# Kernel tuning notes

Measured on AMD Instinct MI355X. Metric: run time of the kernel, lower is better.

## Reference

```python
import jax, jax.numpy as jnp
import numpy as np

HIDDEN = 128
GRID = 8
NB = 32.0            # neighborhood_size
CELL = NB / GRID      # cell_size


def setup_inputs() -> dict:
    key = jax.random.key(0)
    k1, k2, k3, k4 = jax.random.split(key, 4)
    N = 1024
    hidden_states = jax.random.normal(k1, (N, HIDDEN), dtype=jnp.float32)
    positions = jax.random.uniform(k2, (N, 2), dtype=jnp.float32) * 100.0
    fan_in = GRID * GRID * HIDDEN
    bound = 1.0 / np.sqrt(fan_in)
    W = jax.random.uniform(k3, (fan_in, HIDDEN), dtype=jnp.float32, minval=-bound, maxval=bound)
    b = jax.random.uniform(k4, (HIDDEN,), dtype=jnp.float32, minval=-bound, maxval=bound)
    return {"hidden_states": hidden_states, "positions": positions, "W": W, "b": b}


def reference(hidden_states, positions, W, b):
    N, H = hidden_states.shape
    G = GRID
    pos = jax.lax.stop_gradient(positions)  # indices carry no gradient (matches torch int())
    # rel[i, j] = positions[j] - positions[i]
    rel = pos[None, :, :] - pos[:, None, :]                      # [N, N, 2]
    half = NB / 2.0
    inside = (jnp.abs(rel[..., 0]) <= half) & (jnp.abs(rel[..., 1]) <= half)
    not_self = ~jnp.eye(N, dtype=bool)
    valid = inside & not_self                                     # [N, N]
    # rel + half is in [0, NB] when inside, so floor == int() truncation
    gx = jnp.clip(jnp.floor((rel[..., 0] + half) / CELL).astype(jnp.int32), 0, G - 1)
    gy = jnp.clip(jnp.floor((rel[..., 1] + half) / CELL).astype(jnp.int32), 0, G - 1)
    cell = gy * G + gx                                            # [N, N], in [0, G*G)
    # invalid pairs go to a dummy cell G*G per pedestrian
    seg = jnp.where(valid, cell, G * G)
    gid = (jnp.arange(N, dtype=jnp.int32)[:, None] * (G * G + 1) + seg).reshape(-1)
    data = jnp.broadcast_to(hidden_states[None, :, :], (N, N, H)).reshape(N * N, H)
    gmax = jax.ops.segment_max(data, gid, num_segments=N * (G * G + 1))  # [N*(G*G+1), H]
    # torch grid starts at zeros and uses maximum -> clamp at 0; empty cells (-inf) -> 0
    grid = jnp.maximum(gmax.reshape(N, G * G + 1, H)[:, : G * G, :], 0.0)  # [N, G*G, H]
    flat = grid.reshape(N, G * G * H)
    return flat @ W + b
```

## Files before the change

### kernel.cpp

```cpp
#include <hip/hip_runtime.h>
#include <hip/hip_bf16.h>

#define N_PED 1024
#define H 128
#define G 8
#define NCELL 64
#define K_TOT 8192
#define HALF_NB 16.0f
#define INV_CELL 0.25f

#define KSPLIT 16
#define KC 512
#define BM 32
#define BK 64

typedef __attribute__((ext_vector_type(8))) short bf16x8;
typedef __attribute__((ext_vector_type(4))) float f32x4;

__device__ __forceinline__ unsigned map_f2u(float v) {
    unsigned u = __float_as_uint(v);
    return (u & 0x80000000u) ? ~u : (u | 0x80000000u);
}
__device__ __forceinline__ float unmap_u2f(unsigned u) {
    return __uint_as_float((u & 0x80000000u) ? (u ^ 0x80000000u) : ~u);
}
__device__ __forceinline__ ushort f2bf(float f) {
    unsigned u = __float_as_uint(f);
    return (ushort)((u + 0x7FFFu + ((u >> 16) & 1u)) >> 16);
}
__device__ __forceinline__ void gl_lds16(const void* g, void* l) {
    __builtin_amdgcn_global_load_lds(
        (const __attribute__((address_space(1))) void*)g,
        (__attribute__((address_space(3))) void*)l, 16, 0, 0);
}

__global__ __launch_bounds__(512) void fused_pre(const float* __restrict__ hs,
                                                 const float* __restrict__ pos,
                                                 const float* __restrict__ W,
                                                 ushort* __restrict__ grid,
                                                 ushort* __restrict__ Wt) {
    __shared__ __align__(16) char smem[36872];
    const int tid = threadIdx.x;

    if (blockIdx.x < N_PED) {
        unsigned* lgrid = (unsigned*)smem;
        int*      list  = (int*)(smem + 32768);
        int*      cnt   = (int*)(smem + 36864);
        const int i = blockIdx.x;

        const unsigned iu = 0x80000000u;
        uint4 iv = {iu, iu, iu, iu};
        for (int k = tid; k < NCELL * H / 4; k += 512) ((uint4*)lgrid)[k] = iv;
        if (tid == 0) *cnt = 0;
        __syncthreads();

        const float2 pi = ((const float2*)pos)[i];
        for (int j = tid; j < N_PED; j += 512) {
            float2 pj = ((const float2*)pos)[j];
            float rx = pj.x - pi.x;
            float ry = pj.y - pi.y;
            if (j != i && fabsf(rx) <= HALF_NB && fabsf(ry) <= HALF_NB) {
                int gx = (int)floorf((rx + HALF_NB) * INV_CELL);
                int gy = (int)floorf((ry + HALF_NB) * INV_CELL);
                gx = min(G - 1, max(0, gx));
                gy = min(G - 1, max(0, gy));
                int slot = atomicAdd(cnt, 1);
                list[slot] = (j << 8) | (gy * G + gx);
            }
        }
        __syncthreads();

        const int n   = *cnt;
        const int dim = tid & 127;
        const int eg  = tid >> 7;
        for (int e = eg; e < n; e += 4) {
            int packed = list[e];
            int j    = packed >> 8;
            int cell = packed & 255;
            float v = hs[j * H + dim];
            atomicMax(&lgrid[cell * H + dim], map_f2u(v));
        }
        __syncthreads();

        ushort* dst = grid + (size_t)i * K_TOT;
        for (int c = tid; c < K_TOT / 8; c += 512) {
            uint4 a = ((const uint4*)lgrid)[2 * c];
            uint4 b = ((const uint4*)lgrid)[2 * c + 1];
            ushort tmp[8];
            tmp[0] = f2bf(unmap_u2f(a.x)); tmp[1] = f2bf(unmap_u2f(a.y));
            tmp[2] = f2bf(unmap_u2f(a.z)); tmp[3] = f2bf(unmap_u2f(a.w));
            tmp[4] = f2bf(unmap_u2f(b.x)); tmp[5] = f2bf(unmap_u2f(b.y));
            tmp[6] = f2bf(unmap_u2f(b.z)); tmp[7] = f2bf(unmap_u2f(b.w));
            *(bf16x8*)&dst[8 * c] = *(const bf16x8*)tmp;
        }
    } else {
        float* tile = (float*)smem;
        const int bw  = blockIdx.x - N_PED;
        const int k0w = bw * 64;

        for (int x = tid; x < 64 * H; x += 512) {
            int r = x >> 7, c = x & 127;
            tile[r * 129 + c] = W[(size_t)(k0w + r) * H + c];
        }
        __syncthreads();

        const int col = tid >> 2;
        const int kh  = (tid & 3) * 16;
        ushort tmp[16];
        #pragma unroll
        for (int t = 0; t < 16; ++t) tmp[t] = f2bf(tile[(kh + t) * 129 + col]);
        ushort* w0 = Wt + (size_t)col * K_TOT + k0w + kh;
        *(bf16x8*)w0       = *(const bf16x8*)&tmp[0];
        *(bf16x8*)(w0 + 8) = *(const bf16x8*)&tmp[8];
    }
}

__global__ __launch_bounds__(256) void gemm_mfma(const ushort* __restrict__ A,
                                                 const ushort* __restrict__ Wt,
                                                 float* __restrict__ part) {
    __shared__ ushort sA[BM * BK];
    __shared__ ushort sB[H * BK];

    const int m0   = blockIdx.x * BM;
    const int k0   = blockIdx.y * KC;
    const int tid  = threadIdx.x;
    const int wave = tid >> 6;
    const int lane = tid & 63;
    const int ll   = lane & 15;
    const int lh   = lane >> 4;
    const int lr8  = lane >> 3;
    const int cswz = (lane & 7) ^ (lr8 & 7);

    f32x4 acc[2][2] = {};

    for (int kk = 0; kk < KC; kk += BK) {
        const int kcol = k0 + kk;
        gl_lds16(A + (size_t)(m0 + 8 * wave + lr8) * K_TOT + kcol + cswz * 8,
                 &sA[8 * wave * BK]);
        #pragma unroll
        for (int t = 0; t < 4; ++t) {
            int br = 32 * wave + 8 * t;
            gl_lds16(Wt + (size_t)(br + lr8) * K_TOT + kcol + cswz * 8,
                     &sB[br * BK]);
        }
        __syncthreads();

        #pragma unroll
        for (int ks = 0; ks < 2; ++ks) {
            const int chunk = ks * 4 + lh;
            bf16x8 bfrag[2], afrag[2];
            #pragma unroll
            for (int nt = 0; nt < 2; ++nt) {
                int br = wave * 32 + nt * 16 + ll;
                bfrag[nt] = *(const bf16x8*)&sB[br * BK + ((chunk ^ (br & 7)) * 8)];
            }
            #pragma unroll
            for (int mt = 0; mt < 2; ++mt) {
                int ar = mt * 16 + ll;
                afrag[mt] = *(const bf16x8*)&sA[ar * BK + ((chunk ^ (ar & 7)) * 8)];
            }
            #pragma unroll
            for (int mt = 0; mt < 2; ++mt)
                #pragma unroll
                for (int nt = 0; nt < 2; ++nt)
                    acc[mt][nt] = __builtin_amdgcn_mfma_f32_16x16x32_bf16(
                        afrag[mt], bfrag[nt], acc[mt][nt], 0, 0, 0);
        }
        __syncthreads();
    }

    float* dst = part + (size_t)blockIdx.y * (N_PED * H);
    #pragma unroll
    for (int mt = 0; mt < 2; ++mt)
        #pragma unroll
        for (int nt = 0; nt < 2; ++nt) {
            int col   = wave * 32 + nt * 16 + ll;
            int rbase = m0 + mt * 16 + lh * 4;
            #pragma unroll
            for (int r = 0; r < 4; ++r)
                dst[(size_t)(rbase + r) * H + col] = acc[mt][nt][r];
        }
}

__global__ __launch_bounds__(128) void reduce_out(const float* __restrict__ part,
                                                  const float* __restrict__ b,
                                                  float* __restrict__ out) {
    const int idx = (blockIdx.x * 128 + threadIdx.x) * 4;
    float4 acc = *(const float4*)&b[idx & (H - 1)];
    #pragma unroll
    for (int s = 0; s < KSPLIT; ++s) {
        float4 p = *(const float4*)&part[(size_t)s * (N_PED * H) + idx];
        acc.x += p.x; acc.y += p.y; acc.z += p.z; acc.w += p.w;
    }
    *(float4*)&out[idx] = acc;
}

extern "C" void kernel_launch(void* const* d_in, const int* in_sizes, int n_in,
                              void* d_out, int out_size, void* d_ws, size_t ws_size,
                              hipStream_t stream) {
    const float* hs  = (const float*)d_in[0];
    const float* pos = (const float*)d_in[1];
    const float* Wm  = (const float*)d_in[2];
    const float* b   = (const float*)d_in[3];
    float* out = (float*)d_out;

    ushort* grid = (ushort*)d_ws;
    ushort* Wt   = (ushort*)((char*)d_ws + (16u << 20));
    float*  part = (float*)((char*)d_ws + (18u << 20));

    fused_pre<<<N_PED + K_TOT / 64, 512, 0, stream>>>(hs, pos, Wm, grid, Wt);
    gemm_mfma<<<dim3(N_PED / BM, KSPLIT), 256, 0, stream>>>(grid, Wt, part);
    reduce_out<<<(N_PED * H) / (128 * 4), 128, 0, stream>>>(part, b, out);
}
```

Measured before the change: 32.90 us.

## Triple-buffer GEMM LDS loads and vectorize scatter-max with prefetching

The GEMM kernel now keeps three LDS buffers and issues async global-to-LDS loads two K-steps ahead, waiting on vmcnt counters instead of a full barrier after every tile. The aim is to overlap memory latency with MFMA work. Separately, the scatter-max phase now has each thread handle four feature dims with float4 loads and software-prefetches the next neighbor's list entry and hidden-state row. Risks are higher LDS use per block and hand-written waitcnt logic that must stay in step with the number of loads in flight.

```diff
diff --git a/kernel.cpp b/kernel.cpp
--- a/kernel.cpp
+++ b/kernel.cpp
@@ -13,6 +13,7 @@
 #define KC 512
 #define BM 32
 #define BK 64
+#define NSTAGE 8
 
 typedef __attribute__((ext_vector_type(8))) short bf16x8;
 typedef __attribute__((ext_vector_type(4))) float f32x4;
@@ -70,15 +71,24 @@
         }
         __syncthreads();
 
-        const int n   = *cnt;
-        const int dim = tid & 127;
-        const int eg  = tid >> 7;
-        for (int e = eg; e < n; e += 4) {
-            int packed = list[e];
-            int j    = packed >> 8;
-            int cell = packed & 255;
-            float v = hs[j * H + dim];
-            atomicMax(&lgrid[cell * H + dim], map_f2u(v));
+        const int n    = *cnt;
+        const int dim4 = (tid & 31) * 4;
+        const int eg   = tid >> 5;
+        int e  = eg;
+        int p0 = (e < n) ? list[e] : -1;
+        int p1 = (e + 16 < n) ? list[e + 16] : -1;
+        float4 v0 = {};
+        if (p0 >= 0) v0 = *(const float4*)&hs[(p0 >> 8) * H + dim4];
+        while (p0 >= 0) {
+            int p2 = (e + 32 < n) ? list[e + 32] : -1;
+            float4 v1 = {};
+            if (p1 >= 0) v1 = *(const float4*)&hs[(p1 >> 8) * H + dim4];
+            unsigned* gph = &lgrid[(p0 & 255) * H + dim4];
+            atomicMax(gph + 0, map_f2u(v0.x));
+            atomicMax(gph + 1, map_f2u(v0.y));
+            atomicMax(gph + 2, map_f2u(v0.z));
+            atomicMax(gph + 3, map_f2u(v0.w));
+            e += 16; p0 = p1; p1 = p2; v0 = v1;
         }
         __syncthreads();
 
@@ -118,8 +128,8 @@
 __global__ __launch_bounds__(256) void gemm_mfma(const ushort* __restrict__ A,
                                                  const ushort* __restrict__ Wt,
                                                  float* __restrict__ part) {
-    __shared__ ushort sA[BM * BK];
-    __shared__ ushort sB[H * BK];
+    __shared__ ushort sA[3][BM * BK];
+    __shared__ ushort sB[3][H * BK];
 
     const int m0   = blockIdx.x * BM;
     const int k0   = blockIdx.y * KC;
@@ -131,20 +141,30 @@
     const int lr8  = lane >> 3;
     const int cswz = (lane & 7) ^ (lr8 & 7);
 
+    const ushort* Abase = A  + (size_t)(m0 + 8 * wave + lr8) * K_TOT + k0 + cswz * 8;
+    const ushort* Bbase = Wt + (size_t)(32 * wave + lr8) * K_TOT      + k0 + cswz * 8;
+
     f32x4 acc[2][2] = {};
 
-    for (int kk = 0; kk < KC; kk += BK) {
-        const int kcol = k0 + kk;
-        gl_lds16(A + (size_t)(m0 + 8 * wave + lr8) * K_TOT + kcol + cswz * 8,
-                 &sA[8 * wave * BK]);
-        #pragma unroll
-        for (int t = 0; t < 4; ++t) {
-            int br = 32 * wave + 8 * t;
-            gl_lds16(Wt + (size_t)(br + lr8) * K_TOT + kcol + cswz * 8,
-                     &sB[br * BK]);
-        }
-        __syncthreads();
-
+#define STAGE(T, BUF)                                                        \
+    do {                                                                     \
+        gl_lds16(Abase + (T) * BK, &sA[BUF][8 * wave * BK]);                 \
+        gl_lds16(Bbase + (T) * BK,                &sB[BUF][(32 * wave) * BK]);      \
+        gl_lds16(Bbase + (T) * BK +  8 * K_TOT,   &sB[BUF][(32 * wave + 8) * BK]);  \
+        gl_lds16(Bbase + (T) * BK + 16 * K_TOT,   &sB[BUF][(32 * wave + 16) * BK]); \
+        gl_lds16(Bbase + (T) * BK + 24 * K_TOT,   &sB[BUF][(32 * wave + 24) * BK]); \
+    } while (0)
+
+    STAGE(0, 0);
+    STAGE(1, 1);
+    asm volatile("s_waitcnt vmcnt(5)" ::: "memory");
+    __builtin_amdgcn_s_barrier();
+
+    #pragma unroll
+    for (int t = 0; t < NSTAGE; ++t) {
+        if (t + 2 < NSTAGE) STAGE(t + 2, (t + 2) % 3);
+
+        const int buf = t % 3;
         #pragma unroll
         for (int ks = 0; ks < 2; ++ks) {
             const int chunk = ks * 4 + lh;
@@ -152,12 +172,12 @@
             #pragma unroll
             for (int nt = 0; nt < 2; ++nt) {
                 int br = wave * 32 + nt * 16 + ll;
-                bfrag[nt] = *(const bf16x8*)&sB[br * BK + ((chunk ^ (br & 7)) * 8)];
+                bfrag[nt] = *(const bf16x8*)&sB[buf][br * BK + ((chunk ^ (br & 7)) * 8)];
             }
             #pragma unroll
             for (int mt = 0; mt < 2; ++mt) {
                 int ar = mt * 16 + ll;
-                afrag[mt] = *(const bf16x8*)&sA[ar * BK + ((chunk ^ (ar & 7)) * 8)];
+                afrag[mt] = *(const bf16x8*)&sA[buf][ar * BK + ((chunk ^ (ar & 7)) * 8)];
             }
             #pragma unroll
             for (int mt = 0; mt < 2; ++mt)
@@ -166,8 +186,16 @@
                     acc[mt][nt] = __builtin_amdgcn_mfma_f32_16x16x32_bf16(
                         afrag[mt], bfrag[nt], acc[mt][nt], 0, 0, 0);
         }
-        __syncthreads();
+
+        if (t + 1 < NSTAGE) {
+            if (t + 2 < NSTAGE)
+                asm volatile("s_waitcnt vmcnt(5)" ::: "memory");
+            else
+                asm volatile("s_waitcnt vmcnt(0)" ::: "memory");
+            __builtin_amdgcn_s_barrier();
+        }
     }
+#undef STAGE
 
     float* dst = part + (size_t)blockIdx.y * (N_PED * H);
     #pragma unroll
```

Measured after the change: 30.17 us. 8.3% less time.

## Fuse grid max-pooling into GEMM and replace split-K reduction with atomics

Applied to the files above, without the earlier changes.

Rather than building a full bf16 grid tensor in global memory, the prep kernel now only writes per-pedestrian neighbor lists, the bf16 transpose of W, and a bias-initialized output. The GEMM kernel filters each list to its 4-cell K-chunk, builds that slice of the pooled grid in LDS with atomicMax, and runs MFMA with triple-buffered B loads. Results are accumulated into the output with float atomics, which removes the separate reduce kernel, the partial-sum buffer and the 16 MB grid round-trip. In exchange, neighbor lists are capped (256 per pedestrian, 2048 per block), which silently drops neighbors if exceeded. The atomic summation also makes the output order nondeterministic, and the GEMM now needs about 147 KB of LDS per block.

```diff
diff --git a/kernel.cpp b/kernel.cpp
--- a/kernel.cpp
+++ b/kernel.cpp
@@ -4,15 +4,11 @@
 #define N_PED 1024
 #define H 128
 #define G 8
-#define NCELL 64
 #define K_TOT 8192
 #define HALF_NB 16.0f
 #define INV_CELL 0.25f
-
-#define KSPLIT 16
-#define KC 512
-#define BM 32
-#define BK 64
+#define LISTCAP 256
+#define MLISTCAP 2048
 
 typedef __attribute__((ext_vector_type(8))) short bf16x8;
 typedef __attribute__((ext_vector_type(4))) float f32x4;
@@ -34,76 +30,26 @@
         (__attribute__((address_space(3))) void*)l, 16, 0, 0);
 }
 
-__global__ __launch_bounds__(512) void fused_pre(const float* __restrict__ hs,
-                                                 const float* __restrict__ pos,
-                                                 const float* __restrict__ W,
-                                                 ushort* __restrict__ grid,
-                                                 ushort* __restrict__ Wt) {
-    __shared__ __align__(16) char smem[36872];
+__global__ __launch_bounds__(512) void prep(const float* __restrict__ hs,
+                                            const float* __restrict__ pos,
+                                            const float* __restrict__ W,
+                                            const float* __restrict__ b,
+                                            ushort* __restrict__ Wt,
+                                            int* __restrict__ lists,
+                                            int* __restrict__ cntg,
+                                            float* __restrict__ out) {
+    __shared__ __align__(16) char smem[33168];
     const int tid = threadIdx.x;
-
-    if (blockIdx.x < N_PED) {
-        unsigned* lgrid = (unsigned*)smem;
-        int*      list  = (int*)(smem + 32768);
-        int*      cnt   = (int*)(smem + 36864);
-        const int i = blockIdx.x;
-
-        const unsigned iu = 0x80000000u;
-        uint4 iv = {iu, iu, iu, iu};
-        for (int k = tid; k < NCELL * H / 4; k += 512) ((uint4*)lgrid)[k] = iv;
-        if (tid == 0) *cnt = 0;
-        __syncthreads();
-
-        const float2 pi = ((const float2*)pos)[i];
-        for (int j = tid; j < N_PED; j += 512) {
-            float2 pj = ((const float2*)pos)[j];
-            float rx = pj.x - pi.x;
-            float ry = pj.y - pi.y;
-            if (j != i && fabsf(rx) <= HALF_NB && fabsf(ry) <= HALF_NB) {
-                int gx = (int)floorf((rx + HALF_NB) * INV_CELL);
-                int gy = (int)floorf((ry + HALF_NB) * INV_CELL);
-                gx = min(G - 1, max(0, gx));
-                gy = min(G - 1, max(0, gy));
-                int slot = atomicAdd(cnt, 1);
-                list[slot] = (j << 8) | (gy * G + gx);
-            }
-        }
-        __syncthreads();
-
-        const int n   = *cnt;
-        const int dim = tid & 127;
-        const int eg  = tid >> 7;
-        for (int e = eg; e < n; e += 4) {
-            int packed = list[e];
-            int j    = packed >> 8;
-            int cell = packed & 255;
-            float v = hs[j * H + dim];
-            atomicMax(&lgrid[cell * H + dim], map_f2u(v));
-        }
-        __syncthreads();
-
-        ushort* dst = grid + (size_t)i * K_TOT;
-        for (int c = tid; c < K_TOT / 8; c += 512) {
-            uint4 a = ((const uint4*)lgrid)[2 * c];
-            uint4 b = ((const uint4*)lgrid)[2 * c + 1];
-            ushort tmp[8];
-            tmp[0] = f2bf(unmap_u2f(a.x)); tmp[1] = f2bf(unmap_u2f(a.y));
-            tmp[2] = f2bf(unmap_u2f(a.z)); tmp[3] = f2bf(unmap_u2f(a.w));
-            tmp[4] = f2bf(unmap_u2f(b.x)); tmp[5] = f2bf(unmap_u2f(b.y));
-            tmp[6] = f2bf(unmap_u2f(b.z)); tmp[7] = f2bf(unmap_u2f(b.w));
-            *(bf16x8*)&dst[8 * c] = *(const bf16x8*)tmp;
-        }
-    } else {
+    const int bx  = blockIdx.x;
+
+    if (bx < 128) {
         float* tile = (float*)smem;
-        const int bw  = blockIdx.x - N_PED;
-        const int k0w = bw * 64;
-
+        const int k0w = bx * 64;
         for (int x = tid; x < 64 * H; x += 512) {
             int r = x >> 7, c = x & 127;
             tile[r * 129 + c] = W[(size_t)(k0w + r) * H + c];
         }
         __syncthreads();
-
         const int col = tid >> 2;
         const int kh  = (tid & 3) * 16;
         ushort tmp[16];
@@ -112,87 +58,171 @@
         ushort* w0 = Wt + (size_t)col * K_TOT + k0w + kh;
         *(bf16x8*)w0       = *(const bf16x8*)&tmp[0];
         *(bf16x8*)(w0 + 8) = *(const bf16x8*)&tmp[8];
-    }
-}
-
-__global__ __launch_bounds__(256) void gemm_mfma(const ushort* __restrict__ A,
-                                                 const ushort* __restrict__ Wt,
-                                                 float* __restrict__ part) {
-    __shared__ ushort sA[BM * BK];
-    __shared__ ushort sB[H * BK];
-
-    const int m0   = blockIdx.x * BM;
-    const int k0   = blockIdx.y * KC;
-    const int tid  = threadIdx.x;
-    const int wave = tid >> 6;
-    const int lane = tid & 63;
-    const int ll   = lane & 15;
-    const int lh   = lane >> 4;
+    } else if (bx < 160) {
+        float2* pis   = (float2*)smem;
+        int*    lcnt  = (int*)(smem + 256);
+        int*    llist = (int*)(smem + 384);
+        const int base = (bx - 128) * 32;
+        if (tid < 32) { pis[tid] = ((const float2*)pos)[base + tid]; lcnt[tid] = 0; }
+        __syncthreads();
+        for (int j = tid; j < N_PED; j += 512) {
+            float2 pj = ((const float2*)pos)[j];
+            #pragma unroll
+            for (int p = 0; p < 32; ++p) {
+                float rx = pj.x - pis[p].x;
+                float ry = pj.y - pis[p].y;
+                if (j != base + p && fabsf(rx) <= HALF_NB && fabsf(ry) <= HALF_NB) {
+                    int gx = min(G - 1, max(0, (int)floorf((rx + HALF_NB) * INV_CELL)));
+                    int gy = min(G - 1, max(0, (int)floorf((ry + HALF_NB) * INV_CELL)));
+                    int slot = atomicAdd(&lcnt[p], 1);
+                    if (slot < LISTCAP) llist[p * LISTCAP + slot] = (j << 8) | (gy * G + gx);
+                }
+            }
+        }
+        __syncthreads();
+        for (int x = tid; x < 32 * 64; x += 512)
+            ((int4*)lists)[base * 64 + x] = ((const int4*)llist)[x];
+        if (tid < 32) cntg[base + tid] = min(lcnt[tid], LISTCAP);
+    } else {
+        const float4* b4 = (const float4*)b;
+        float4* out4 = (float4*)out;
+        const int b0 = (bx - 160) * 16384;
+        for (int i = tid; i < 16384; i += 512) {
+            int g = b0 + i;
+            out4[g] = b4[g & 31];
+        }
+    }
+}
+
+__global__ __launch_bounds__(512) void gemm_fused(const float* __restrict__ hs,
+                                                  const ushort* __restrict__ Wt,
+                                                  const int* __restrict__ lists,
+                                                  const int* __restrict__ cntg,
+                                                  float* __restrict__ out) {
+    __shared__ __align__(16) char smem[147600];
+    ushort* Alds  = (ushort*)smem;
+    int*    mlist = (int*)smem;
+    uint*   P     = (uint*)(smem + 32768);
+    ushort* Blds  = (ushort*)(smem + 98304);
+    int*    mcnt  = (int*)(smem + 147456);
+    int*    scnt  = (int*)(smem + 147460);
+
+    const int tid = threadIdx.x;
+    const int m0  = blockIdx.x * 32;
+    const int cy  = blockIdx.y;
+
+    const int wave = tid >> 6, lane = tid & 63;
+    const int ll = lane & 15, lh = lane >> 4;
     const int lr8  = lane >> 3;
     const int cswz = (lane & 7) ^ (lr8 & 7);
-
-    f32x4 acc[2][2] = {};
-
-    for (int kk = 0; kk < KC; kk += BK) {
-        const int kcol = k0 + kk;
-        gl_lds16(A + (size_t)(m0 + 8 * wave + lr8) * K_TOT + kcol + cswz * 8,
-                 &sA[8 * wave * BK]);
-        #pragma unroll
-        for (int t = 0; t < 4; ++t) {
-            int br = 32 * wave + 8 * t;
-            gl_lds16(Wt + (size_t)(br + lr8) * K_TOT + kcol + cswz * 8,
-                     &sB[br * BK]);
-        }
-        __syncthreads();
-
+    const ushort* B0 = Wt + (size_t)(16 * wave + lr8) * K_TOT + cy * 512 + cswz * 8;
+
+#define STAGE(T, BUF)                                                         \
+    do {                                                                      \
+        gl_lds16(B0 + (T) * 64,             Blds + (BUF) * 8192 + (16 * wave) * 64);     \
+        gl_lds16(B0 + (T) * 64 + 8 * K_TOT, Blds + (BUF) * 8192 + (16 * wave + 8) * 64); \
+    } while (0)
+
+    STAGE(0, 0);
+    STAGE(1, 1);
+
+    {
+        uint4 iv = {0x80000000u, 0x80000000u, 0x80000000u, 0x80000000u};
+        uint4* P4 = (uint4*)P;
+        for (int i = tid; i < 4096; i += 512) P4[i] = iv;
+        if (tid == 0) *mcnt = 0;
+        if (tid < 32) scnt[tid] = cntg[m0 + tid];
+    }
+    __syncthreads();
+
+    for (int x = tid; x < 32 * 64; x += 512) {
+        int p = x >> 6, q = x & 63;
+        int4 v = ((const int4*)(lists + (size_t)(m0 + p) * LISTCAP))[q];
+        int n = scnt[p];
+        int e0 = q * 4;
+        int vv[4] = {v.x, v.y, v.z, v.w};
+        #pragma unroll
+        for (int i = 0; i < 4; ++i) {
+            if (e0 + i < n) {
+                int pk = vv[i];
+                int cell = pk & 255;
+                if ((cell >> 2) == cy) {
+                    int slot = atomicAdd(mcnt, 1);
+                    if (slot < MLISTCAP)
+                        mlist[slot] = ((pk >> 8) << 7) | (p << 2) | (cell & 3);
+                }
+            }
+        }
+    }
+    __syncthreads();
+
+    const int mc = min(*mcnt, MLISTCAP);
+    const float4* hs4 = (const float4*)hs;
+    for (int u = tid; u < mc * 32; u += 512) {
+        int m = u >> 5, f = u & 31;
+        int pk = mlist[m];
+        int j = pk >> 7, p = (pk >> 2) & 31, c = pk & 3;
+        float4 v = hs4[j * 32 + f];
+        uint* q = P + p * 512 + c * 128 + f * 4;
+        atomicMax(q + 0, map_f2u(v.x));
+        atomicMax(q + 1, map_f2u(v.y));
+        atomicMax(q + 2, map_f2u(v.z));
+        atomicMax(q + 3, map_f2u(v.w));
+    }
+    __syncthreads();
+
+    for (int x = tid; x < 2048; x += 512) {
+        int r = x >> 6, c = x & 63;
+        const uint* src = P + r * 512 + c * 8;
+        ushort tmp[8];
+        #pragma unroll
+        for (int i = 0; i < 8; ++i) tmp[i] = f2bf(unmap_u2f(src[i]));
+        *(bf16x8*)&Alds[r * 512 + (c ^ (r & 7)) * 8] = *(const bf16x8*)tmp;
+    }
+
+    const int mt = wave >> 2;
+    const int nq = wave & 3;
+
+    f32x4 acc[2] = {};
+
+    asm volatile("s_waitcnt vmcnt(2)" ::: "memory");
+    __syncthreads();
+
+    #pragma unroll
+    for (int t = 0; t < 8; ++t) {
+        if (t + 2 < 8) STAGE(t + 2, (t + 2) % 3);
+        const ushort* Bb = Blds + (t % 3) * 8192;
         #pragma unroll
         for (int ks = 0; ks < 2; ++ks) {
-            const int chunk = ks * 4 + lh;
-            bf16x8 bfrag[2], afrag[2];
+            int ch  = ks * 4 + lh;
+            int gch = t * 8 + ch;
+            bf16x8 bfrag[2];
             #pragma unroll
             for (int nt = 0; nt < 2; ++nt) {
-                int br = wave * 32 + nt * 16 + ll;
-                bfrag[nt] = *(const bf16x8*)&sB[br * BK + ((chunk ^ (br & 7)) * 8)];
+                int br = nq * 32 + nt * 16 + ll;
+                bfrag[nt] = *(const bf16x8*)&Bb[br * 64 + ((ch ^ (br & 7)) * 8)];
             }
-            #pragma unroll
-            for (int mt = 0; mt < 2; ++mt) {
-                int ar = mt * 16 + ll;
-                afrag[mt] = *(const bf16x8*)&sA[ar * BK + ((chunk ^ (ar & 7)) * 8)];
-            }
-            #pragma unroll
-            for (int mt = 0; mt < 2; ++mt)
-                #pragma unroll
-                for (int nt = 0; nt < 2; ++nt)
-                    acc[mt][nt] = __builtin_amdgcn_mfma_f32_16x16x32_bf16(
-                        afrag[mt], bfrag[nt], acc[mt][nt], 0, 0, 0);
-        }
-        __syncthreads();
-    }
-
-    float* dst = part + (size_t)blockIdx.y * (N_PED * H);
+            int ar = mt * 16 + ll;
+            bf16x8 afrag = *(const bf16x8*)&Alds[ar * 512 + ((gch ^ (ar & 7)) * 8)];
+            acc[0] = __builtin_amdgcn_mfma_f32_16x16x32_bf16(afrag, bfrag[0], acc[0], 0, 0, 0);
+            acc[1] = __builtin_amdgcn_mfma_f32_16x16x32_bf16(afrag, bfrag[1], acc[1], 0, 0, 0);
+        }
+        if (t + 1 < 8) {
+            if (t + 2 < 8) asm volatile("s_waitcnt vmcnt(2)" ::: "memory");
+            else           asm volatile("s_waitcnt vmcnt(0)" ::: "memory");
+            __builtin_amdgcn_s_barrier();
+        }
+    }
+#undef STAGE
+
     #pragma unroll
-    for (int mt = 0; mt < 2; ++mt)
-        #pragma unroll
-        for (int nt = 0; nt < 2; ++nt) {
-            int col   = wave * 32 + nt * 16 + ll;
-            int rbase = m0 + mt * 16 + lh * 4;
-            #pragma unroll
-            for (int r = 0; r < 4; ++r)
-                dst[(size_t)(rbase + r) * H + col] = acc[mt][nt][r];
-        }
-}
-
-__global__ __launch_bounds__(128) void reduce_out(const float* __restrict__ part,
-                                                  const float* __restrict__ b,
-                                                  float* __restrict__ out) {
-    const int idx = (blockIdx.x * 128 + threadIdx.x) * 4;
-    float4 acc = *(const float4*)&b[idx & (H - 1)];
-    #pragma unroll
-    for (int s = 0; s < KSPLIT; ++s) {
-        float4 p = *(const float4*)&part[(size_t)s * (N_PED * H) + idx];
-        acc.x += p.x; acc.y += p.y; acc.z += p.z; acc.w += p.w;
-    }
-    *(float4*)&out[idx] = acc;
+    for (int nt = 0; nt < 2; ++nt) {
+        int col = nq * 32 + nt * 16 + ll;
+        int row = m0 + mt * 16 + lh * 4;
+        #pragma unroll
+        for (int r = 0; r < 4; ++r)
+            atomicAdd(&out[(size_t)(row + r) * H + col], acc[nt][r]);
+    }
 }
 
 extern "C" void kernel_launch(void* const* d_in, const int* in_sizes, int n_in,
@@ -204,11 +234,10 @@
     const float* b   = (const float*)d_in[3];
     float* out = (float*)d_out;
 
-    ushort* grid = (ushort*)d_ws;
-    ushort* Wt   = (ushort*)((char*)d_ws + (16u << 20));
-    float*  part = (float*)((char*)d_ws + (18u << 20));
-
-    fused_pre<<<N_PED + K_TOT / 64, 512, 0, stream>>>(hs, pos, Wm, grid, Wt);
-    gemm_mfma<<<dim3(N_PED / BM, KSPLIT), 256, 0, stream>>>(grid, Wt, part);
-    reduce_out<<<(N_PED * H) / (128 * 4), 128, 0, stream>>>(part, b, out);
-}
+    ushort* Wt    = (ushort*)d_ws;
+    int*    lists = (int*)((char*)d_ws + (2u << 20));
+    int*    cntg  = (int*)((char*)d_ws + (3u << 20));
+
+    prep<<<162, 512, 0, stream>>>(hs, pos, Wm, b, Wt, lists, cntg, out);
+    gemm_fused<<<dim3(32, 16), 512, 0, stream>>>(hs, Wt, lists, cntg, out);
+}
```

Result: slower. 41.97 us (+27.6%).
